# Optimization experiments

Measured on AMD Instinct MI355X. Metric: run time of the kernel, lower is better.

The kernel has to match this reference:

```python
import jax, jax.numpy as jnp
import numpy as np

D_MODEL = 2048
NUM_HEADS = 16
HEAD_DIM = 128


def setup_inputs() -> dict:
    key = jax.random.key(0)
    ks = jax.random.split(key, 9)
    B, S = 2, 2048
    s_in = 1.0 / np.sqrt(D_MODEL)
    return {
        "x": jax.random.normal(ks[0], (B, S, D_MODEL), dtype=jnp.float32),
        "wq": jax.random.normal(ks[1], (D_MODEL, D_MODEL), dtype=jnp.float32) * s_in,
        "bq": jnp.zeros((D_MODEL,), jnp.float32),
        "wk": jax.random.normal(ks[2], (D_MODEL, HEAD_DIM), dtype=jnp.float32) * s_in,
        "bk": jnp.zeros((HEAD_DIM,), jnp.float32),
        "wv": jax.random.normal(ks[3], (D_MODEL, HEAD_DIM), dtype=jnp.float32) * s_in,
        "bv": jnpp_zeros(ks) if False else jnp.zeros((HEAD_DIM,), jnp.float32),
        "wo": jax.random.normal(ks[4], (D_MODEL, D_MODEL), dtype=jnp.float32) * s_in,
        "bo": jnp.zeros((D_MODEL,), jnp.float32),
    }


def reference(x, wq, bq, wk, bk, wv, bv, wo, bo):
    B, S, _ = x.shape
    H, Dh = NUM_HEADS, HEAD_DIM
    q = (x @ wq + bq).reshape(B, S, H, Dh)          # [B,S,H,Dh]
    k = x @ wk + bk                                  # [B,S,Dh] (single KV head)
    v = x @ wv + bv                                  # [B,S,Dh]
    scale = 1.0 / jnp.sqrt(jnp.asarray(Dh, x.dtype))
    # scores: [B,H,Sq,Sk] — MQA: K shared across heads
    scores = jnp.einsum('bqhd,bkd->bhqk', q, k) * scale
    attn = jax.nn.softmax(scores, axis=-1)
    out = jnp.einsum('bhqk,bkd->bqhd', attn, v).reshape(B, S, H * Dh)
    return out @ wo + bo
```

## Files before the change

kernel.cpp:

```cpp
#include <hip/hip_runtime.h>
#include <stdint.h>

typedef unsigned short u16;

#define D_MODEL 2048
#define HEADS 16
#define HDIM 128
#define SEQ 2048
#define BATCH 2
#define NROWS (BATCH*SEQ)
#define QKV_N (D_MODEL + 2*HDIM)

typedef __attribute__((ext_vector_type(8))) short bf16x8;
typedef __attribute__((ext_vector_type(4))) float f32x4;

__device__ inline u16 f2bf(float f) {
  union { float f; uint32_t u; } v; v.f = f;
  uint32_t r = v.u + 0x7FFFu + ((v.u >> 16) & 1u);
  return (u16)(r >> 16);
}
__device__ inline u16 f2bf_fast(float f) {
  union { float f; uint32_t u; } v; v.f = f;
  return (u16)((v.u + 0x8000u) >> 16);
}

__device__ inline void gload_lds16(const void* g, void* l) {
  __builtin_amdgcn_global_load_lds(
      (const __attribute__((address_space(1))) unsigned int*)g,
      (__attribute__((address_space(3))) unsigned int*)l, 16, 0, 0);
}

__global__ void cvt_bf16_4(const float* __restrict__ s, u16* __restrict__ d, int n4) {
  int i = blockIdx.x * 256 + threadIdx.x;
  if (i < n4) {
    float4 f = ((const float4*)s)[i];
    ushort4 u;
    u.x = f2bf(f.x); u.y = f2bf(f.y); u.z = f2bf(f.z); u.w = f2bf(f.w);
    ((ushort4*)d)[i] = u;
  }
}

__global__ void transpose_cvt(const float* __restrict__ src, u16* __restrict__ dst,
                              int N, int dstOff) {
  __shared__ float t[32][33];
  const int k0 = blockIdx.y * 32, n0 = blockIdx.x * 32;
  const int tx = threadIdx.x, ty = threadIdx.y;
#pragma unroll
  for (int i = 0; i < 4; i++)
    t[ty + 8*i][tx] = src[(size_t)(k0 + ty + 8*i) * N + n0 + tx];
  __syncthreads();
#pragma unroll
  for (int i = 0; i < 4; i++)
    dst[(size_t)(dstOff + n0 + ty + 8*i) * D_MODEL + k0 + tx] = f2bf(t[tx][ty + 8*i]);
}

__global__ void pack_bias(const float* __restrict__ bq, const float* __restrict__ bk,
                          const float* __restrict__ bv, float* __restrict__ o) {
  int i = blockIdx.x * 256 + threadIdx.x;
  if (i < QKV_N)
    o[i] = (i < D_MODEL) ? bq[i] : ((i < D_MODEL + HDIM) ? bk[i - D_MODEL] : bv[i - D_MODEL - HDIM]);
}

#define BM 128
#define BN 128
#define BK 32

__global__ __launch_bounds__(256) void gemm_bt(
    const u16* __restrict__ A, const u16* __restrict__ BT,
    const float* __restrict__ bias,
    u16* __restrict__ Cb, float* __restrict__ Cf,
    u16* __restrict__ vT,
    int M, int N, int K, int tilesN) {
  __shared__ __align__(16) u16 sA[BM * BK];
  __shared__ __align__(16) u16 sB[BN * BK];
  const int tid = threadIdx.x;
  const int wave = tid >> 6, lane = tid & 63;
  const int bm = blockIdx.x / tilesN, bn = blockIdx.x % tilesN;
  const int m0 = bm * BM, n0 = bn * BN;
  const int wm = (wave & 1) * 64, wn = (wave >> 1) * 64;
  const int l16 = lane & 15, kq = (lane >> 4) * 8;

  f32x4 acc[4][4] = {};
  const int srow = lane >> 2, scol = (lane & 3) * 8;

  for (int k0 = 0; k0 < K; k0 += BK) {
    __syncthreads();
#pragma unroll
    for (int c = 0; c < 2; c++) {
      const int chunk = wave * 2 + c;
      const int row = chunk * 16 + srow;
      gload_lds16(&A[(size_t)(m0 + row) * K + k0 + scol], &sA[chunk * 512]);
      gload_lds16(&BT[(size_t)(n0 + row) * K + k0 + scol], &sB[chunk * 512]);
    }
    __syncthreads();
    bf16x8 af[4], bfr[4];
#pragma unroll
    for (int mb = 0; mb < 4; ++mb) af[mb]  = *(const bf16x8*)&sA[(wm + mb*16 + l16) * BK + kq];
#pragma unroll
    for (int nb = 0; nb < 4; ++nb) bfr[nb] = *(const bf16x8*)&sB[(wn + nb*16 + l16) * BK + kq];
#pragma unroll
    for (int mb = 0; mb < 4; ++mb)
#pragma unroll
      for (int nb = 0; nb < 4; ++nb)
        acc[mb][nb] = __builtin_amdgcn_mfma_f32_16x16x32_bf16(af[mb], bfr[nb], acc[mb][nb], 0, 0, 0);
  }

#pragma unroll
  for (int mb = 0; mb < 4; ++mb) {
#pragma unroll
    for (int nb = 0; nb < 4; ++nb) {
      const int gn = n0 + wn + nb * 16 + l16;
      const float bb = bias ? bias[gn] : 0.0f;
#pragma unroll
      for (int r = 0; r < 4; ++r) {
        const int gm = m0 + wm + mb * 16 + (lane >> 4) * 4 + r;
        const float v = acc[mb][nb][r] + bb;
        if (Cf) {
          Cf[(size_t)gm * N + gn] = v;
        } else {
          const u16 u = f2bf(v);
          Cb[(size_t)gm * N + gn] = u;
          if (vT && gn >= D_MODEL + HDIM) {
            const int bi = gm >> 11, si = gm & 2047;
            vT[((size_t)bi * HDIM + (gn - D_MODEL - HDIM)) * SEQ + si] = u;
          }
        }
      }
    }
  }
}

__global__ __launch_bounds__(256) void mqa_attn(
    const u16* __restrict__ qkv, const u16* __restrict__ vT, u16* __restrict__ ctx) {
  __shared__ __align__(16) u16 sK[2][64 * 128];
  __shared__ __align__(16) u16 sV[128 * 64];
  __shared__ __align__(16) u16 sP[4][32 * 64];
  const int tid = threadIdx.x, wave = tid >> 6, lane = tid & 63;
  const int qt = blockIdx.x & 15;
  const int h  = (blockIdx.x >> 4) & 15;
  const int b  = blockIdx.x >> 8;
  const int bS = b * SEQ;
  const int q0 = qt * 128 + wave * 32;
  const int l16 = lane & 15, quad = lane >> 4;
  const int sw = l16 & 7;
  u16* myP = &sP[wave][0];

  bf16x8 qf[2][4];
#pragma unroll
  for (int mb = 0; mb < 2; mb++)
#pragma unroll
    for (int kc = 0; kc < 4; kc++)
      qf[mb][kc] = *(const bf16x8*)&qkv[(size_t)(bS + q0 + mb*16 + l16) * QKV_N
                                        + h*HDIM + kc*32 + quad*8];

  f32x4 o[2][8] = {};
  float lrow[2] = {0.f, 0.f};
  const float sc2 = 0.08838834764831845f * 1.4426950408889634f;

  const u16* Kbase = qkv + (size_t)bS * QKV_N + D_MODEL;
  const u16* Vbase = vT + (size_t)b * HDIM * SEQ;

  const int kRowIn = lane >> 4;
  const int kChS   = lane & 15;
  const int vRowIn = lane >> 3;
  const int vChL   = (lane & 7) ^ (lane >> 3);

#define DMA_K(t, dst)                                                          \
  {                                                                            \
    const int _sk = (t) * 64;                                                  \
    _Pragma("unroll") for (int j = 0; j < 4; j++) {                            \
      const int i = wave * 4 + j;                                              \
      const int krow = i * 4 + kRowIn;                                         \
      const int kcl = kChS ^ (krow & 15);                                      \
      gload_lds16(&Kbase[(size_t)(_sk + krow) * QKV_N + kcl * 8],              \
                  &(dst)[i * 512]);                                            \
    }                                                                          \
  }
#define DMA_V(t)                                                               \
  {                                                                            \
    const int _sk = (t) * 64;                                                  \
    _Pragma("unroll") for (int j = 0; j < 4; j++) {                            \
      const int i = wave * 4 + j;                                              \
      const int d = i * 8 + vRowIn;                                            \
      gload_lds16(&Vbase[(size_t)d * SEQ + _sk + vChL * 8], &sV[i * 512]);     \
    }                                                                          \
  }

  DMA_K(0, sK[0]);
  DMA_V(0);
  __syncthreads();

  const int T = SEQ / 64;
  for (int t = 0; t < T; ++t) {
    const int cur = t & 1;
    if (t + 1 < T) DMA_K(t + 1, sK[cur ^ 1]);

    f32x4 sc[2][4];
#pragma unroll
    for (int nb = 0; nb < 4; nb++) {
      bf16x8 kf[4];
#pragma unroll
      for (int kc = 0; kc < 4; kc++)
        kf[kc] = *(const bf16x8*)&sK[cur][(nb*16 + l16) * 128 + (((kc*4 + quad) ^ l16) * 8)];
#pragma unroll
      for (int mb = 0; mb < 2; mb++) {
        f32x4 a = {0.f, 0.f, 0.f, 0.f};
#pragma unroll
        for (int kc = 0; kc < 4; kc++)
          a = __builtin_amdgcn_mfma_f32_16x16x32_bf16(kf[kc], qf[mb][kc], a, 0, 0, 0);
        sc[mb][nb] = a;
      }
    }

#pragma unroll
    for (int mb = 0; mb < 2; mb++)
#pragma unroll
      for (int nb = 0; nb < 4; nb++) {
        float p0 = __builtin_amdgcn_exp2f(sc[mb][nb][0] * sc2);
        float p1 = __builtin_amdgcn_exp2f(sc[mb][nb][1] * sc2);
        float p2 = __builtin_amdgcn_exp2f(sc[mb][nb][2] * sc2);
        float p3 = __builtin_amdgcn_exp2f(sc[mb][nb][3] * sc2);
        lrow[mb] += (p0 + p1) + (p2 + p3);
        uint32_t lo = (uint32_t)f2bf_fast(p0) | ((uint32_t)f2bf_fast(p1) << 16);
        uint32_t hi = (uint32_t)f2bf_fast(p2) | ((uint32_t)f2bf_fast(p3) << 16);
        uint2 w; w.x = lo; w.y = hi;
        const int pr = (nb*2 + (quad >> 1)) ^ sw;
        *(uint2*)&myP[(mb*16 + l16) * 64 + pr * 8 + (quad & 1) * 4] = w;
      }

    __syncthreads();

    bf16x8 pf[2][2];
#pragma unroll
    for (int mb = 0; mb < 2; mb++)
#pragma unroll
      for (int kc = 0; kc < 2; kc++)
        pf[mb][kc] = *(const bf16x8*)&myP[(mb*16 + l16) * 64 + (((kc*4 + quad) ^ sw) * 8)];
#pragma unroll
    for (int nb = 0; nb < 8; nb++) {
      bf16x8 vf[2];
#pragma unroll
      for (int kc = 0; kc < 2; kc++)
        vf[kc] = *(const bf16x8*)&sV[(nb*16 + l16) * 64 + (((kc*4 + quad) ^ (l16 & 7)) * 8)];
#pragma unroll
      for (int mb = 0; mb < 2; mb++)
#pragma unroll
        for (int kc = 0; kc < 2; kc++)
          o[mb][nb] = __builtin_amdgcn_mfma_f32_16x16x32_bf16(pf[mb][kc], vf[kc], o[mb][nb], 0, 0, 0);
    }

    __syncthreads();
    if (t + 1 < T) DMA_V(t + 1);
  }

#pragma unroll
  for (int mb = 0; mb < 2; mb++) {
    lrow[mb] += __shfl_xor(lrow[mb], 16, 64);
    lrow[mb] += __shfl_xor(lrow[mb], 32, 64);
  }
  float invl[2][4];
#pragma unroll
  for (int mb = 0; mb < 2; mb++)
#pragma unroll
    for (int r = 0; r < 4; r++)
      invl[mb][r] = 1.0f / __shfl(lrow[mb], quad * 4 + r, 64);

#pragma unroll
  for (int mb = 0; mb < 2; mb++)
#pragma unroll
    for (int nb = 0; nb < 8; nb++)
#pragma unroll
      for (int r = 0; r < 4; r++) {
        const int gq = q0 + mb*16 + quad*4 + r;
        const int gd = h * HDIM + nb*16 + l16;
        ctx[(size_t)(bS + gq) * D_MODEL + gd] = f2bf(o[mb][nb][r] * invl[mb][r]);
      }
}

extern "C" void kernel_launch(void* const* d_in, const int* in_sizes, int n_in,
                              void* d_out, int out_size, void* d_ws, size_t ws_size,
                              hipStream_t stream) {
  const float* x  = (const float*)d_in[0];
  const float* wq = (const float*)d_in[1];
  const float* bq = (const float*)d_in[2];
  const float* wk = (const float*)d_in[3];
  const float* bk = (const float*)d_in[4];
  const float* wv = (const float*)d_in[5];
  const float* bv = (const float*)d_in[6];
  const float* wo = (const float*)d_in[7];
  const float* bo = (const float*)d_in[8];
  float* out = (float*)d_out;
  char* ws = (char*)d_ws;

  u16*   xb    = (u16*)(ws + 0);
  u16*   wqkvT = (u16*)(ws + 16777216);
  u16*   woT   = (u16*)(ws + 26214400);
  u16*   qkv   = (u16*)(ws + 34603008);
  u16*   vT    = (u16*)(ws + 53477376);
  u16*   ctx   = (u16*)(ws + 54525952);
  float* biasq = (float*)(ws + 71303168);

  cvt_bf16_4<<<8192, 256, 0, stream>>>(x, xb, (NROWS * D_MODEL) / 4);
  dim3 tb(32, 8);
  transpose_cvt<<<dim3(64, 64), tb, 0, stream>>>(wq, wqkvT, 2048, 0);
  transpose_cvt<<<dim3(4, 64),  tb, 0, stream>>>(wk, wqkvT, 128, 2048);
  transpose_cvt<<<dim3(4, 64),  tb, 0, stream>>>(wv, wqkvT, 128, 2176);
  transpose_cvt<<<dim3(64, 64), tb, 0, stream>>>(wo, woT, 2048, 0);
  pack_bias<<<9, 256, 0, stream>>>(bq, bk, bv, biasq);

  gemm_bt<<<32 * 18, 256, 0, stream>>>(xb, wqkvT, biasq, qkv, nullptr, vT,
                                       NROWS, QKV_N, D_MODEL, 18);
  mqa_attn<<<BATCH * HEADS * (SEQ / 128), 256, 0, stream>>>(qkv, vT, ctx);
  gemm_bt<<<32 * 16, 256, 0, stream>>>(ctx, woT, bo, nullptr, out, nullptr,
                                       NROWS, D_MODEL, D_MODEL, 16);
}
```

Before: 334.0 us.

## Double-buffer GEMM LDS loads, merge prep kernels, split QKV GEMM launch

The GEMM now uses two LDS buffers and issues the next K-tile's global-to-LDS loads before computing the current one, so each iteration needs one barrier instead of two. The activation convert is merged with bias packing, and the four weight transposes are merged into one launch, which cuts kernel launches. The QKV projection is split into a Q GEMM and a separate small K/V GEMM, so only the second one takes the vT-write path. There is a possible race: a single barrier per iteration may let the async LDS load into the other buffer overlap with waves still reading it, and the small KV launch of 64 blocks underfills the GPU.

New measurement: 350.8 us. +5.0%, slower.

```diff
diff --git a/kernel.cpp b/kernel.cpp
--- a/kernel.cpp
+++ b/kernel.cpp
@@ -30,20 +30,33 @@
       (__attribute__((address_space(3))) unsigned int*)l, 16, 0, 0);
 }
 
-__global__ void cvt_bf16_4(const float* __restrict__ s, u16* __restrict__ d, int n4) {
-  int i = blockIdx.x * 256 + threadIdx.x;
-  if (i < n4) {
+__global__ void cvt_bias(const float* __restrict__ s, u16* __restrict__ d,
+                         const float* __restrict__ bq, const float* __restrict__ bk,
+                         const float* __restrict__ bv, float* __restrict__ biasq) {
+  const int bid = blockIdx.x;
+  if (bid < 8192) {
+    int i = bid * 256 + threadIdx.x;
     float4 f = ((const float4*)s)[i];
     ushort4 u;
     u.x = f2bf(f.x); u.y = f2bf(f.y); u.z = f2bf(f.z); u.w = f2bf(f.w);
     ((ushort4*)d)[i] = u;
-  }
-}
-
-__global__ void transpose_cvt(const float* __restrict__ src, u16* __restrict__ dst,
-                              int N, int dstOff) {
+  } else {
+    for (int i = threadIdx.x; i < QKV_N; i += 256)
+      biasq[i] = (i < D_MODEL) ? bq[i]
+               : ((i < D_MODEL + HDIM) ? bk[i - D_MODEL] : bv[i - D_MODEL - HDIM]);
+  }
+}
+
+__global__ void transpose_all(const float* __restrict__ wq, const float* __restrict__ wk,
+                              const float* __restrict__ wv, const float* __restrict__ wo,
+                              u16* __restrict__ wqkvT, u16* __restrict__ woT) {
   __shared__ float t[32][33];
-  const int k0 = blockIdx.y * 32, n0 = blockIdx.x * 32;
+  const int n0v = blockIdx.x * 32, k0 = blockIdx.y * 32;
+  const float* src; int N, n0, drow; u16* dst;
+  if (n0v < 2048)      { src = wq; N = 2048; n0 = n0v;        dst = wqkvT; drow = n0v; }
+  else if (n0v < 2176) { src = wk; N = 128;  n0 = n0v - 2048; dst = wqkvT; drow = n0v; }
+  else if (n0v < 2304) { src = wv; N = 128;  n0 = n0v - 2176; dst = wqkvT; drow = n0v; }
+  else                 { src = wo; N = 2048; n0 = n0v - 2304; dst = woT;   drow = n0v - 2304; }
   const int tx = threadIdx.x, ty = threadIdx.y;
 #pragma unroll
   for (int i = 0; i < 4; i++)
@@ -51,14 +64,7 @@
   __syncthreads();
 #pragma unroll
   for (int i = 0; i < 4; i++)
-    dst[(size_t)(dstOff + n0 + ty + 8*i) * D_MODEL + k0 + tx] = f2bf(t[tx][ty + 8*i]);
-}
-
-__global__ void pack_bias(const float* __restrict__ bq, const float* __restrict__ bk,
-                          const float* __restrict__ bv, float* __restrict__ o) {
-  int i = blockIdx.x * 256 + threadIdx.x;
-  if (i < QKV_N)
-    o[i] = (i < D_MODEL) ? bq[i] : ((i < D_MODEL + HDIM) ? bk[i - D_MODEL] : bv[i - D_MODEL - HDIM]);
+    dst[(size_t)(drow + ty + 8*i) * D_MODEL + k0 + tx] = f2bf(t[tx][ty + 8*i]);
 }
 
 #define BM 128
@@ -70,9 +76,9 @@
     const float* __restrict__ bias,
     u16* __restrict__ Cb, float* __restrict__ Cf,
     u16* __restrict__ vT,
-    int M, int N, int K, int tilesN) {
-  __shared__ __align__(16) u16 sA[BM * BK];
-  __shared__ __align__(16) u16 sB[BN * BK];
+    int M, int Nld, int colOff, int tilesN, int K) {
+  __shared__ __align__(16) u16 sA[2][BM * BK];
+  __shared__ __align__(16) u16 sB[2][BN * BK];
   const int tid = threadIdx.x;
   const int wave = tid >> 6, lane = tid & 63;
   const int bm = blockIdx.x / tilesN, bn = blockIdx.x % tilesN;
@@ -83,43 +89,54 @@
   f32x4 acc[4][4] = {};
   const int srow = lane >> 2, scol = (lane & 3) * 8;
 
-  for (int k0 = 0; k0 < K; k0 += BK) {
+#define GDMA(i, buf)                                                           \
+  {                                                                            \
+    const int _k0 = (i) * BK;                                                  \
+    _Pragma("unroll") for (int c = 0; c < 2; c++) {                            \
+      const int chunk = wave * 2 + c;                                          \
+      const int row = chunk * 16 + srow;                                       \
+      gload_lds16(&A[(size_t)(m0 + row) * K + _k0 + scol],                     \
+                  &sA[buf][chunk * 512]);                                      \
+      gload_lds16(&BT[(size_t)(n0 + row) * K + _k0 + scol],                    \
+                  &sB[buf][chunk * 512]);                                      \
+    }                                                                          \
+  }
+
+  const int NI = K / BK;
+  GDMA(0, 0);
+  for (int i = 0; i < NI; i++) {
+    const int cur = i & 1;
     __syncthreads();
-#pragma unroll
-    for (int c = 0; c < 2; c++) {
-      const int chunk = wave * 2 + c;
-      const int row = chunk * 16 + srow;
-      gload_lds16(&A[(size_t)(m0 + row) * K + k0 + scol], &sA[chunk * 512]);
-      gload_lds16(&BT[(size_t)(n0 + row) * K + k0 + scol], &sB[chunk * 512]);
-    }
-    __syncthreads();
+    if (i + 1 < NI) GDMA(i + 1, cur ^ 1);
     bf16x8 af[4], bfr[4];
 #pragma unroll
-    for (int mb = 0; mb < 4; ++mb) af[mb]  = *(const bf16x8*)&sA[(wm + mb*16 + l16) * BK + kq];
-#pragma unroll
-    for (int nb = 0; nb < 4; ++nb) bfr[nb] = *(const bf16x8*)&sB[(wn + nb*16 + l16) * BK + kq];
+    for (int mb = 0; mb < 4; ++mb) af[mb]  = *(const bf16x8*)&sA[cur][(wm + mb*16 + l16) * BK + kq];
+#pragma unroll
+    for (int nb = 0; nb < 4; ++nb) bfr[nb] = *(const bf16x8*)&sB[cur][(wn + nb*16 + l16) * BK + kq];
 #pragma unroll
     for (int mb = 0; mb < 4; ++mb)
 #pragma unroll
       for (int nb = 0; nb < 4; ++nb)
         acc[mb][nb] = __builtin_amdgcn_mfma_f32_16x16x32_bf16(af[mb], bfr[nb], acc[mb][nb], 0, 0, 0);
   }
+#undef GDMA
 
 #pragma unroll
   for (int mb = 0; mb < 4; ++mb) {
 #pragma unroll
     for (int nb = 0; nb < 4; ++nb) {
-      const int gn = n0 + wn + nb * 16 + l16;
-      const float bb = bias ? bias[gn] : 0.0f;
+      const int gnL = n0 + wn + nb * 16 + l16;
+      const int gn = colOff + gnL;
+      const float bb = bias ? bias[gnL] : 0.0f;
 #pragma unroll
       for (int r = 0; r < 4; ++r) {
         const int gm = m0 + wm + mb * 16 + (lane >> 4) * 4 + r;
         const float v = acc[mb][nb][r] + bb;
         if (Cf) {
-          Cf[(size_t)gm * N + gn] = v;
+          Cf[(size_t)gm * Nld + gn] = v;
         } else {
           const u16 u = f2bf(v);
-          Cb[(size_t)gm * N + gn] = u;
+          Cb[(size_t)gm * Nld + gn] = u;
           if (vT && gn >= D_MODEL + HDIM) {
             const int bi = gm >> 11, si = gm & 2047;
             vT[((size_t)bi * HDIM + (gn - D_MODEL - HDIM)) * SEQ + si] = u;
@@ -300,17 +317,15 @@
   u16*   ctx   = (u16*)(ws + 54525952);
   float* biasq = (float*)(ws + 71303168);
 
-  cvt_bf16_4<<<8192, 256, 0, stream>>>(x, xb, (NROWS * D_MODEL) / 4);
-  dim3 tb(32, 8);
-  transpose_cvt<<<dim3(64, 64), tb, 0, stream>>>(wq, wqkvT, 2048, 0);
-  transpose_cvt<<<dim3(4, 64),  tb, 0, stream>>>(wk, wqkvT, 128, 2048);
-  transpose_cvt<<<dim3(4, 64),  tb, 0, stream>>>(wv, wqkvT, 128, 2176);
-  transpose_cvt<<<dim3(64, 64), tb, 0, stream>>>(wo, woT, 2048, 0);
-  pack_bias<<<9, 256, 0, stream>>>(bq, bk, bv, biasq);
-
-  gemm_bt<<<32 * 18, 256, 0, stream>>>(xb, wqkvT, biasq, qkv, nullptr, vT,
-                                       NROWS, QKV_N, D_MODEL, 18);
+  cvt_bias<<<8193, 256, 0, stream>>>(x, xb, bq, bk, bv, biasq);
+  transpose_all<<<dim3(136, 64), dim3(32, 8), 0, stream>>>(wq, wk, wv, wo, wqkvT, woT);
+
+  gemm_bt<<<32 * 16, 256, 0, stream>>>(xb, wqkvT, biasq, qkv, nullptr, nullptr,
+                                       NROWS, QKV_N, 0, 16, D_MODEL);
+  gemm_bt<<<32 * 2, 256, 0, stream>>>(xb, wqkvT + (size_t)D_MODEL * D_MODEL,
+                                      biasq + D_MODEL, qkv, nullptr, vT,
+                                      NROWS, QKV_N, D_MODEL, 2, D_MODEL);
   mqa_attn<<<BATCH * HEADS * (SEQ / 128), 256, 0, stream>>>(qkv, vT, ctx);
   gemm_bt<<<32 * 16, 256, 0, stream>>>(ctx, woT, bo, nullptr, out, nullptr,
-                                       NROWS, D_MODEL, D_MODEL, 16);
-}
+                                       NROWS, D_MODEL, 0, 16, D_MODEL);
+}
```
